# Kernel tuning notes

Hardware: AMD Instinct MI355X
Metric: run time of the kernel (lower is better)

Reference implementation:

```python
import jax, jax.numpy as jnp
import numpy as np

N = 65536   # nodes
D = 64      # feature dim
K = 32      # top-k kept features per node (k_value)
DEG = 16    # average degree
E = N * DEG # edges


def setup_inputs() -> dict:
    key = jax.random.key(0)
    k1, k2, k3, k4, k5 = jax.random.split(key, 5)
    feat = jax.random.normal(k1, (N, D), dtype=jnp.float32)
    topk_values = jax.random.normal(k2, (N, K), dtype=jnp.float32)
    topk_indices = jax.random.randint(k3, (N, K), 0, D, dtype=jnp.int32)
    edge_src = jax.random.randint(k4, (E,), 0, N, dtype=jnp.int32)
    # sorted dst row ids == CSR row structure (expanded indptr)
    edge_dst = jnp.sort(jax.random.randint(k5, (E,), 0, N, dtype=jnp.int32))
    eps = jnp.zeros((1,), dtype=jnp.float32)  # init_eps=0, learn_eps=False
    return {"feat": feat, "topk_values": topk_values, "eps": eps,
            "topk_indices": topk_indices, "edge_src": edge_src, "edge_dst": edge_dst}


def reference(feat, topk_values, eps, topk_indices, edge_src, edge_dst):
    n, d = feat.shape
    # MaxK SpMM: reconstruct sparse (top-k compressed) dense features, then
    # CSR sum-aggregation with unit edge values (graph_values = ones).
    rows = jnp.arange(n, dtype=topk_indices.dtype)[:, None]        # [N,1]
    dense = jnp.zeros_like(feat).at[rows, topk_indices].add(topk_values)  # [N,D]
    # neigh[i] = sum_{j in N(i)} dense[j]
    neigh = jax.ops.segment_sum(dense[edge_src], edge_dst, num_segments=n)  # [N,D]
    # GIN update: (1 + eps) * feat_dst + neigh  (apply_func=None, activation=None)
    return (1.0 + eps) * feat + neigh
```

## Files before the change

### kernel.cpp

```cpp
#include <hip/hip_runtime.h>


#define DFEAT 64
#define KTOP  32

__global__ __launch_bounds__(256) void build_dense_kernel(
    const float* __restrict__ topk_v,
    const int*   __restrict__ topk_i,
    float*       __restrict__ dense,
    int n_nodes)
{
    __shared__ float rows[4][DFEAT];
    int wid  = threadIdx.x >> 6;
    int lane = threadIdx.x & 63;
    int wave = (blockIdx.x * blockDim.x + threadIdx.x) >> 6;
    bool active = wave < n_nodes;

    if (active) rows[wid][lane] = 0.0f;
    __syncthreads();
    if (active && lane < KTOP) {
        int   idx = topk_i[wave * KTOP + lane];
        float val = topk_v[wave * KTOP + lane];
        atomicAdd(&rows[wid][idx], val);
    }
    __syncthreads();
    if (active) dense[(size_t)wave * DFEAT + lane] = rows[wid][lane];
}

__global__ __launch_bounds__(256) void build_indptr_kernel(
    const int* __restrict__ edge_dst,
    int*       __restrict__ indptr,
    int n_nodes, int n_edges)
{
    int e = blockIdx.x * blockDim.x + threadIdx.x;
    if (e >= n_edges) return;
    int cur  = edge_dst[e];
    int prev = (e == 0) ? -1 : edge_dst[e - 1];
    for (int node = prev + 1; node <= cur; ++node) indptr[node] = e;
    if (e == n_edges - 1) {
        for (int node = cur + 1; node <= n_nodes; ++node) indptr[node] = n_edges;
    }
}

__global__ __launch_bounds__(256) void aggregate_kernel(
    const float4* __restrict__ dense4,
    const float4* __restrict__ feat4,
    const float*  __restrict__ eps,
    const int*    __restrict__ edge_src,
    const int*    __restrict__ edge_dst,
    const int*    __restrict__ indptr,
    float4*       __restrict__ out4,
    int n_nodes, int n_edges)
{
    int wave = (blockIdx.x * blockDim.x + threadIdx.x) >> 6;
    int lane = threadIdx.x & 63;
    if (wave >= n_nodes) return;
    int f  = lane & 15;
    int eg = lane >> 4;

    int start, end;
    if (indptr) {
        start = indptr[wave];
        end   = indptr[wave + 1];
    } else {
        int lo = 0, hi = n_edges;
        while (lo < hi) { int mid = (lo + hi) >> 1; if (edge_dst[mid] < wave) lo = mid + 1; else hi = mid; }
        start = lo; hi = n_edges;
        while (lo < hi) { int mid = (lo + hi) >> 1; if (edge_dst[mid] <= wave) lo = mid + 1; else hi = mid; }
        end = lo;
    }

    float4 acc = make_float4(0.f, 0.f, 0.f, 0.f);
    for (int base = start; base < end; base += 8) {
        int e0 = base + eg;
        int e1 = base + 4 + eg;
        if (e0 < end) {
            int s0 = edge_src[e0];
            float4 r0 = dense4[(size_t)s0 * 16 + f];
            acc.x += r0.x; acc.y += r0.y; acc.z += r0.z; acc.w += r0.w;
        }
        if (e1 < end) {
            int s1 = edge_src[e1];
            float4 r1 = dense4[(size_t)s1 * 16 + f];
            acc.x += r1.x; acc.y += r1.y; acc.z += r1.z; acc.w += r1.w;
        }
    }

    acc.x += __shfl_xor(acc.x, 16, 64);
    acc.y += __shfl_xor(acc.y, 16, 64);
    acc.z += __shfl_xor(acc.z, 16, 64);
    acc.w += __shfl_xor(acc.w, 16, 64);
    acc.x += __shfl_xor(acc.x, 32, 64);
    acc.y += __shfl_xor(acc.y, 32, 64);
    acc.z += __shfl_xor(acc.z, 32, 64);
    acc.w += __shfl_xor(acc.w, 32, 64);

    if (eg == 0) {
        float  sc = 1.0f + eps[0];
        float4 ft = feat4[(size_t)wave * 16 + f];
        float4 o;
        o.x = sc * ft.x + acc.x;
        o.y = sc * ft.y + acc.y;
        o.z = sc * ft.z + acc.z;
        o.w = sc * ft.w + acc.w;
        out4[(size_t)wave * 16 + f] = o;
    }
}

extern "C" void kernel_launch(void* const* d_in, const int* in_sizes, int n_in,
                              void* d_out, int out_size, void* d_ws, size_t ws_size,
                              hipStream_t stream)
{
    const float* feat     = (const float*)d_in[0];
    const float* topk_v   = (const float*)d_in[1];
    const float* eps      = (const float*)d_in[2];
    const int*   topk_i   = (const int*)d_in[3];
    const int*   edge_src = (const int*)d_in[4];
    const int*   edge_dst = (const int*)d_in[5];
    float*       out      = (float*)d_out;

    int n_nodes = in_sizes[0] / DFEAT;
    int n_edges = in_sizes[4];

    float* dense = (float*)d_ws;
    size_t dense_bytes = (size_t)n_nodes * DFEAT * sizeof(float);
    int*   indptr = nullptr;
    if (ws_size >= dense_bytes + (size_t)(n_nodes + 1) * sizeof(int))
        indptr = (int*)((char*)d_ws + dense_bytes);

    int node_blocks = (n_nodes + 3) / 4;
    build_dense_kernel<<<node_blocks, 256, 0, stream>>>(topk_v, topk_i, dense, n_nodes);
    if (indptr) {
        int edge_blocks = (n_edges + 255) / 256;
        build_indptr_kernel<<<edge_blocks, 256, 0, stream>>>(edge_dst, indptr, n_nodes, n_edges);
    }
    aggregate_kernel<<<node_blocks, 256, 0, stream>>>(
        (const float4*)dense, (const float4*)feat, eps, edge_src, edge_dst,
        indptr, (float4*)out, n_nodes, n_edges);
}
```

Before: 145.8 us.

## Fuse dense and indptr build into one persistent prep kernel; grid-stride aggregation

Merges the dense-reconstruction and CSR indptr kernels into a single grid-stride prep kernel, saving one launch. Dense rows are now built with wave shuffles and a compare-select instead of shared-memory atomics. Both kernels now use fixed persistent grids (1024 and 2048 blocks) that loop over nodes. The binary-search fallback and the workspace-size check are removed, so indptr is assumed to always fit in the workspace.

```diff
diff --git a/kernel.cpp b/kernel.cpp
--- a/kernel.cpp
+++ b/kernel.cpp
@@ -4,41 +4,44 @@
 #define DFEAT 64
 #define KTOP  32
 
-__global__ __launch_bounds__(256) void build_dense_kernel(
+__global__ __launch_bounds__(256) void prep_kernel(
     const float* __restrict__ topk_v,
     const int*   __restrict__ topk_i,
+    const int*   __restrict__ edge_dst,
     float*       __restrict__ dense,
-    int n_nodes)
-{
-    __shared__ float rows[4][DFEAT];
-    int wid  = threadIdx.x >> 6;
-    int lane = threadIdx.x & 63;
-    int wave = (blockIdx.x * blockDim.x + threadIdx.x) >> 6;
-    bool active = wave < n_nodes;
-
-    if (active) rows[wid][lane] = 0.0f;
-    __syncthreads();
-    if (active && lane < KTOP) {
-        int   idx = topk_i[wave * KTOP + lane];
-        float val = topk_v[wave * KTOP + lane];
-        atomicAdd(&rows[wid][idx], val);
-    }
-    __syncthreads();
-    if (active) dense[(size_t)wave * DFEAT + lane] = rows[wid][lane];
-}
-
-__global__ __launch_bounds__(256) void build_indptr_kernel(
-    const int* __restrict__ edge_dst,
-    int*       __restrict__ indptr,
+    int*         __restrict__ indptr,
     int n_nodes, int n_edges)
 {
-    int e = blockIdx.x * blockDim.x + threadIdx.x;
-    if (e >= n_edges) return;
-    int cur  = edge_dst[e];
-    int prev = (e == 0) ? -1 : edge_dst[e - 1];
-    for (int node = prev + 1; node <= cur; ++node) indptr[node] = e;
-    if (e == n_edges - 1) {
-        for (int node = cur + 1; node <= n_nodes; ++node) indptr[node] = n_edges;
+    int tid      = blockIdx.x * blockDim.x + threadIdx.x;
+    int nthreads = gridDim.x * blockDim.x;
+
+    for (int e = tid; e < n_edges; e += nthreads) {
+        int cur  = edge_dst[e];
+        int prev = (e == 0) ? -1 : edge_dst[e - 1];
+        for (int node = prev + 1; node <= cur; ++node) indptr[node] = e;
+        if (e == n_edges - 1) {
+            for (int node = cur + 1; node <= n_nodes; ++node) indptr[node] = n_edges;
+        }
+    }
+
+    int lane   = threadIdx.x & 63;
+    int wave   = tid >> 6;
+    int nwaves = nthreads >> 6;
+    for (int node = wave; node < n_nodes; node += nwaves) {
+        int   idx = -1;
+        float val = 0.0f;
+        if (lane < KTOP) {
+            idx = topk_i[node * KTOP + lane];
+            val = topk_v[node * KTOP + lane];
+        }
+        float acc = 0.0f;
+#pragma unroll
+        for (int k = 0; k < KTOP; ++k) {
+            int   ik = __shfl(idx, k, 64);
+            float vk = __shfl(val, k, 64);
+            acc += (ik == lane) ? vk : 0.0f;
+        }
+        dense[(size_t)node * DFEAT + lane] = acc;
     }
 }
 
@@ -47,63 +50,55 @@
     const float4* __restrict__ feat4,
     const float*  __restrict__ eps,
     const int*    __restrict__ edge_src,
-    const int*    __restrict__ edge_dst,
     const int*    __restrict__ indptr,
     float4*       __restrict__ out4,
-    int n_nodes, int n_edges)
+    int n_nodes)
 {
-    int wave = (blockIdx.x * blockDim.x + threadIdx.x) >> 6;
-    int lane = threadIdx.x & 63;
-    if (wave >= n_nodes) return;
-    int f  = lane & 15;
-    int eg = lane >> 4;
+    int lane   = threadIdx.x & 63;
+    int f      = lane & 15;
+    int eg     = lane >> 4;
+    int wave   = (blockIdx.x * blockDim.x + threadIdx.x) >> 6;
+    int nwaves = (gridDim.x * blockDim.x) >> 6;
+    float sc   = 1.0f + eps[0];
 
-    int start, end;
-    if (indptr) {
-        start = indptr[wave];
-        end   = indptr[wave + 1];
-    } else {
-        int lo = 0, hi = n_edges;
-        while (lo < hi) { int mid = (lo + hi) >> 1; if (edge_dst[mid] < wave) lo = mid + 1; else hi = mid; }
-        start = lo; hi = n_edges;
-        while (lo < hi) { int mid = (lo + hi) >> 1; if (edge_dst[mid] <= wave) lo = mid + 1; else hi = mid; }
-        end = lo;
-    }
+    for (int node = wave; node < n_nodes; node += nwaves) {
+        int start = indptr[node];
+        int end   = indptr[node + 1];
 
-    float4 acc = make_float4(0.f, 0.f, 0.f, 0.f);
-    for (int base = start; base < end; base += 8) {
-        int e0 = base + eg;
-        int e1 = base + 4 + eg;
-        if (e0 < end) {
-            int s0 = edge_src[e0];
-            float4 r0 = dense4[(size_t)s0 * 16 + f];
-            acc.x += r0.x; acc.y += r0.y; acc.z += r0.z; acc.w += r0.w;
+        float4 acc = make_float4(0.f, 0.f, 0.f, 0.f);
+        for (int base = start; base < end; base += 8) {
+            int e0 = base + eg;
+            int e1 = base + 4 + eg;
+            if (e0 < end) {
+                int s0 = edge_src[e0];
+                float4 r0 = dense4[(size_t)s0 * 16 + f];
+                acc.x += r0.x; acc.y += r0.y; acc.z += r0.z; acc.w += r0.w;
+            }
+            if (e1 < end) {
+                int s1 = edge_src[e1];
+                float4 r1 = dense4[(size_t)s1 * 16 + f];
+                acc.x += r1.x; acc.y += r1.y; acc.z += r1.z; acc.w += r1.w;
+            }
         }
-        if (e1 < end) {
-            int s1 = edge_src[e1];
-            float4 r1 = dense4[(size_t)s1 * 16 + f];
-            acc.x += r1.x; acc.y += r1.y; acc.z += r1.z; acc.w += r1.w;
+
+        acc.x += __shfl_xor(acc.x, 16, 64);
+        acc.y += __shfl_xor(acc.y, 16, 64);
+        acc.z += __shfl_xor(acc.z, 16, 64);
+        acc.w += __shfl_xor(acc.w, 16, 64);
+        acc.x += __shfl_xor(acc.x, 32, 64);
+        acc.y += __shfl_xor(acc.y, 32, 64);
+        acc.z += __shfl_xor(acc.z, 32, 64);
+        acc.w += __shfl_xor(acc.w, 32, 64);
+
+        if (eg == 0) {
+            float4 ft = feat4[(size_t)node * 16 + f];
+            float4 o;
+            o.x = sc * ft.x + acc.x;
+            o.y = sc * ft.y + acc.y;
+            o.z = sc * ft.z + acc.z;
+            o.w = sc * ft.w + acc.w;
+            out4[(size_t)node * 16 + f] = o;
         }
-    }
-
-    acc.x += __shfl_xor(acc.x, 16, 64);
-    acc.y += __shfl_xor(acc.y, 16, 64);
-    acc.z += __shfl_xor(acc.z, 16, 64);
-    acc.w += __shfl_xor(acc.w, 16, 64);
-    acc.x += __shfl_xor(acc.x, 32, 64);
-    acc.y += __shfl_xor(acc.y, 32, 64);
-    acc.z += __shfl_xor(acc.z, 32, 64);
-    acc.w += __shfl_xor(acc.w, 32, 64);
-
-    if (eg == 0) {
-        float  sc = 1.0f + eps[0];
-        float4 ft = feat4[(size_t)wave * 16 + f];
-        float4 o;
-        o.x = sc * ft.x + acc.x;
-        o.y = sc * ft.y + acc.y;
-        o.z = sc * ft.z + acc.z;
-        o.w = sc * ft.w + acc.w;
-        out4[(size_t)wave * 16 + f] = o;
     }
 }
 
@@ -124,17 +119,11 @@
 
     float* dense = (float*)d_ws;
     size_t dense_bytes = (size_t)n_nodes * DFEAT * sizeof(float);
-    int*   indptr = nullptr;
-    if (ws_size >= dense_bytes + (size_t)(n_nodes + 1) * sizeof(int))
-        indptr = (int*)((char*)d_ws + dense_bytes);
+    int*   indptr = (int*)((char*)d_ws + dense_bytes);
 
-    int node_blocks = (n_nodes + 3) / 4;
-    build_dense_kernel<<<node_blocks, 256, 0, stream>>>(topk_v, topk_i, dense, n_nodes);
-    if (indptr) {
-        int edge_blocks = (n_edges + 255) / 256;
-        build_indptr_kernel<<<edge_blocks, 256, 0, stream>>>(edge_dst, indptr, n_nodes, n_edges);
-    }
-    aggregate_kernel<<<node_blocks, 256, 0, stream>>>(
-        (const float4*)dense, (const float4*)feat, eps, edge_src, edge_dst,
-        indptr, (float4*)out, n_nodes, n_edges);
+    prep_kernel<<<1024, 256, 0, stream>>>(topk_v, topk_i, edge_dst,
+                                          dense, indptr, n_nodes, n_edges);
+    aggregate_kernel<<<2048, 256, 0, stream>>>(
+        (const float4*)dense, (const float4*)feat, eps, edge_src,
+        indptr, (float4*)out, n_nodes);
 }
```

After: 172.6 us. 1.18x slower.
